# Kernel tuning notes

Hardware: AMD Instinct MI355X
Metric: run time of the kernel (lower is better)

The kernel has to match this reference:

```python
import jax, jax.numpy as jnp
import numpy as np

B, S, D, H = 2, 2048, 1024, 16
HD = D // H  # 64


def setup_inputs() -> dict:
    key = jax.random.key(0)
    ks = jax.random.split(key, 10)
    inp = {
        "queries": jax.random.normal(ks[0], (B, S, D), dtype=jnp.float32),
        "keys": jax.random.normal(ks[1], (B, S, D), dtype=jnp.float32),
        "values": jax.random.normal(ks[2], (B, S, D), dtype=jnp.float32),
        "attention_mask": jax.random.randint(ks[3], (B, S), 0, 2, dtype=jnp.int32),
        # Linear params (torch nn.Linear: y = x @ W.T + b), scaled like default init
        "Wq": jax.random.normal(ks[4], (D, D), dtype=jnp.float32) / np.sqrt(D),
        "bq": jnp.zeros((D,), dtype=jnp.float32),
        "Wk": jax.random.normal(ks[5], (D, D), dtype=jnp.float32) / np.sqrt(D),
        "bk": jnp.zeros((D,), dtype=jnp.float32),
        "Wv": jax.random.normal(ks[6], (D, D), dtype=jnp.float32) / np.sqrt(D),
        "bv": jnp.zeros((D,), dtype=jnp.float32),
    }
    return inp


def _split_heads(x):
    # torch.chunk along last dim + stack(dim=1) == reshape + transpose
    b, s, d = x.shape
    return x.reshape(b, s, H, HD).transpose(0, 2, 1, 3)  # [B,H,S,hd]


def reference(queries, keys, values, attention_mask, Wq, bq, Wk, bk, Wv, bv):
    q = jax.nn.relu(queries @ Wq.T + bq)
    k = jax.nn.relu(keys @ Wk.T + bk)
    v = jax.nn.relu(values @ Wv.T + bv)
    qh, kh, vh = _split_heads(q), _split_heads(k), _split_heads(v)
    score = jnp.einsum("bhqd,bhkd->bhqk", qh, kh) / jnp.sqrt(jnp.float32(HD))
    # enc mask: [B,1,S,1] broadcast over key dim — masks whole query rows where mask==0
    row_mask = (attention_mask == 0)[:, None, :, None]
    score = jnp.where(row_mask, jnp.float32(-1e9), score)
    attn = jax.nn.softmax(score, axis=-1)
    a = jnp.einsum("bhqk,bhkd->bhqd", attn, vh)  # [B,H,S,hd]
    # faithful to original: permute(0,1,3,2) then reshape to (B,S,D)
    a = a.transpose(0, 1, 3, 2).reshape(q.shape[0], q.shape[1], q.shape[2])
    return a + queries
```

## Files before the change

### kernel.cpp

```cpp
#include <hip/hip_runtime.h>
#include <hip/hip_bf16.h>

#define DEV __device__ __forceinline__

typedef __attribute__((ext_vector_type(8))) short short8;
typedef __attribute__((ext_vector_type(4))) float f32x4;

#define MFMA16(a, b, c) __builtin_amdgcn_mfma_f32_16x16x32_bf16((a), (b), (c), 0, 0, 0)

static constexpr int B_ = 2, S_ = 2048, D_ = 1024, H_ = 16, HD_ = 64;
static constexpr long NX = (long)B_ * S_ * D_;
static constexpr long NW = (long)D_ * D_;

DEV short f2bf(float f) {
    __hip_bfloat16 h = __float2bfloat16(f);
    union { __hip_bfloat16 hh; short s; } u;
    u.hh = h;
    return u.s;
}

DEV float bf2f(short s) {
    union { float f; unsigned u; } x;
    x.u = ((unsigned)(unsigned short)s) << 16;
    return x.f;
}

DEV short8 ld8(const short* p) { return *(const short8*)p; }

DEV void gld16(const short* g, short* l) {
    __builtin_amdgcn_global_load_lds(
        (const __attribute__((address_space(1))) unsigned int*)g,
        (__attribute__((address_space(3))) unsigned int*)l, 16, 0, 0);
}

__global__ __launch_bounds__(256) void convert_all(
    const float* __restrict__ q, const float* __restrict__ k, const float* __restrict__ v,
    const float* __restrict__ wq, const float* __restrict__ wk, const float* __restrict__ wv,
    short* __restrict__ qb, short* __restrict__ kb, short* __restrict__ vb,
    short* __restrict__ wqb, short* __restrict__ wkb, short* __restrict__ wvb) {
    long tid = (long)blockIdx.x * 256 + threadIdx.x;
    long e = tid * 4;
    const float* src; short* dst; long off;
    if      (e < NX)            { src = q;  dst = qb;  off = e; }
    else if (e < 2*NX)          { src = k;  dst = kb;  off = e - NX; }
    else if (e < 3*NX)          { src = v;  dst = vb;  off = e - 2*NX; }
    else if (e < 3*NX + NW)     { src = wq; dst = wqb; off = e - 3*NX; }
    else if (e < 3*NX + 2*NW)   { src = wk; dst = wkb; off = e - 3*NX - NW; }
    else                        { src = wv; dst = wvb; off = e - 3*NX - 2*NW; }
    float4 f = *(const float4*)(src + off);
    short4 o;
    o.x = f2bf(f.x); o.y = f2bf(f.y); o.z = f2bf(f.z); o.w = f2bf(f.w);
    *(short4*)(dst + off) = o;
}

__global__ __launch_bounds__(256) void gemm_bias_relu(
    const short* __restrict__ X0, const short* __restrict__ X1, const short* __restrict__ X2,
    const short* __restrict__ W0, const short* __restrict__ W1, const short* __restrict__ W2,
    const float* __restrict__ b0, const float* __restrict__ b1, const float* __restrict__ b2,
    short* __restrict__ O0, short* __restrict__ O1, short* __restrict__ O2) {
    __shared__ short As[2][128 * 32];
    __shared__ short Bs[2][128 * 32];

    const int z = blockIdx.z;
    const short* X   = (z == 0) ? X0 : (z == 1) ? X1 : X2;
    const short* W   = (z == 0) ? W0 : (z == 1) ? W1 : W2;
    const float* bia = (z == 0) ? b0 : (z == 1) ? b1 : b2;
    short*       Out = (z == 0) ? O0 : (z == 1) ? O1 : O2;

    const int tid  = threadIdx.x;
    const int wid  = tid >> 6;
    const int lane = tid & 63;
    const int id   = lane & 15;
    const int quad = lane >> 4;
    const int m0 = blockIdx.y * 128;
    const int n0 = blockIdx.x * 128;
    const int wm = (wid >> 1) * 64;
    const int wn = (wid & 1) * 64;

    const short* Ag0 = X + (long)(m0 + wid * 32 + (lane >> 2)) * D_ + (lane & 3) * 8;
    const short* Bg0 = W + (long)(n0 + wid * 32 + (lane >> 2)) * D_ + (lane & 3) * 8;
    const int offW = wid * 1024;

    f32x4 acc[4][4] = {};

    gld16(Ag0,            &As[0][offW]);
    gld16(Ag0 + 16 * D_,  &As[0][offW + 512]);
    gld16(Bg0,            &Bs[0][offW]);
    gld16(Bg0 + 16 * D_,  &Bs[0][offW + 512]);

    for (int kk = 0; kk < D_; kk += 32) {
        const int cur = (kk >> 5) & 1;
        __syncthreads();
        if (kk + 32 < D_) {
            const int nxt = cur ^ 1;
            gld16(Ag0 + kk + 32,            &As[nxt][offW]);
            gld16(Ag0 + 16 * D_ + kk + 32,  &As[nxt][offW + 512]);
            gld16(Bg0 + kk + 32,            &Bs[nxt][offW]);
            gld16(Bg0 + 16 * D_ + kk + 32,  &Bs[nxt][offW + 512]);
        }

        short8 af[4], bf[4];
#pragma unroll
        for (int i = 0; i < 4; i++) af[i] = ld8(&As[cur][(wm + 16*i + id) * 32 + quad * 8]);
#pragma unroll
        for (int j = 0; j < 4; j++) bf[j] = ld8(&Bs[cur][(wn + 16*j + id) * 32 + quad * 8]);
#pragma unroll
        for (int i = 0; i < 4; i++)
#pragma unroll
            for (int j = 0; j < 4; j++)
                acc[i][j] = MFMA16(af[i], bf[j], acc[i][j]);
    }

#pragma unroll
    for (int j = 0; j < 4; j++) {
        int col = n0 + wn + 16*j + id;
        float bj = bia[col];
#pragma unroll
        for (int i = 0; i < 4; i++) {
#pragma unroll
            for (int r = 0; r < 4; r++) {
                int row = m0 + wm + 16*i + quad*4 + r;
                float val = fmaxf(acc[i][j][r] + bj, 0.f);
                Out[(long)row * D_ + col] = f2bf(val);
            }
        }
    }
}

__global__ __launch_bounds__(256) void transpose_v(const short* __restrict__ Vp,
                                                   short* __restrict__ VT) {
    __shared__ short tile[64 * 64];
    const int bh = blockIdx.y;
    const int b = bh >> 4, h = bh & 15;
    const int s0 = blockIdx.x * 64;
    const int t = threadIdx.x;
#pragma unroll
    for (int it = 0; it < 2; it++) {
        int row = (t >> 3) + 32 * it;
        int u   = t & 7;
        short8 d = ld8(Vp + (long)(b * S_ + s0 + row) * D_ + h * HD_ + u * 8);
        *(short8*)(&tile[row * 64 + (u ^ ((row >> 3) & 7)) * 8]) = d;
    }
    __syncthreads();
#pragma unroll
    for (int it = 0; it < 2; it++) {
        int e  = (t >> 3) + 32 * it;
        int sb = (t & 7) * 8;
        short8 o;
#pragma unroll
        for (int u = 0; u < 8; u++) {
            int row = sb + u;
            o[u] = tile[row * 64 + (((e >> 3) ^ ((row >> 3) & 7)) * 8) + (e & 7)];
        }
        *(short8*)(VT + ((long)bh * HD_ + e) * S_ + s0 + sb) = o;
    }
}

__global__ __launch_bounds__(256, 2) void attention(
    const short* __restrict__ Qb, const short* __restrict__ Kb,
    const short* __restrict__ VT, const int* __restrict__ mask,
    const float* __restrict__ queries, float* __restrict__ out) {
    __shared__ short Ks[2][64 * 64];
    __shared__ short Vs[2][64 * 64];
    __shared__ short pl[4][2 * 16 * 72];

    const int tid  = threadIdx.x;
    const int wid  = tid >> 6;
    const int lane = tid & 63;
    const int id   = lane & 15;
    const int quad = lane >> 4;

    const int bid = blockIdx.x;
    const int qb_ = bid & 15;
    const int h   = (bid >> 4) & 15;
    const int b   = bid >> 8;
    const int q0  = qb_ * 128 + wid * 32;

    short8 qf[2][2];
#pragma unroll
    for (int g = 0; g < 2; g++) {
        const short* qbase = Qb + (long)(b * S_ + q0 + g * 16 + id) * D_ + h * HD_ + quad * 8;
        short8 f0 = ld8(qbase);
        short8 f1 = ld8(qbase + 32);
        const float qsc = mask[b * S_ + q0 + g * 16 + id] ? 0.125f : 0.f;
#pragma unroll
        for (int i = 0; i < 8; i++) {
            f0[i] = f2bf(bf2f(f0[i]) * qsc);
            f1[i] = f2bf(bf2f(f1[i]) * qsc);
        }
        qf[g][0] = f0; qf[g][1] = f1;
    }

    const int srow = wid * 16 + (lane >> 3);
    const int su   = (lane & 7) ^ (srow & 7);
    const short* kg0 = Kb + ((long)b * S_ + srow) * D_ + h * HD_ + su * 8;
    const short* vg0 = VT + (((long)(b * H_ + h) * HD_) + srow) * S_ + su * 8;
    short* plw = pl[wid];

    const int swz = id & 7;

    float l4[2][4] = {};
    f32x4 o[2][4] = {};

    gld16(kg0,            &Ks[0][wid * 1024]);
    gld16(kg0 + 8 * D_,   &Ks[0][wid * 1024 + 512]);
    gld16(vg0,            &Vs[0][wid * 1024]);
    gld16(vg0 + 8 * S_,   &Vs[0][wid * 1024 + 512]);

    for (int c0 = 0; c0 < S_; c0 += 64) {
        const int cur = (c0 >> 6) & 1;
        __syncthreads();
        if (c0 + 64 < S_) {
            const int nxt = cur ^ 1;
            const long cg = (long)(c0 + 64);
            gld16(kg0 + cg * D_,           &Ks[nxt][wid * 1024]);
            gld16(kg0 + cg * D_ + 8 * D_,  &Ks[nxt][wid * 1024 + 512]);
            gld16(vg0 + cg,                &Vs[nxt][wid * 1024]);
            gld16(vg0 + cg + 8 * S_,       &Vs[nxt][wid * 1024 + 512]);
        }

        f32x4 s[2][4];
#pragma unroll
        for (int g = 0; g < 2; g++)
#pragma unroll
            for (int t = 0; t < 4; t++) s[g][t] = (f32x4){0.f, 0.f, 0.f, 0.f};
#pragma unroll
        for (int t = 0; t < 4; t++) {
            short8 a0 = ld8(&Ks[cur][(16*t + id) * 64 + ((quad    ) ^ swz) * 8]);
            short8 a1 = ld8(&Ks[cur][(16*t + id) * 64 + ((quad ^ 4) ^ swz) * 8]);
            s[0][t] = MFMA16(a0, qf[0][0], s[0][t]);
            s[0][t] = MFMA16(a1, qf[0][1], s[0][t]);
            s[1][t] = MFMA16(a0, qf[1][0], s[1][t]);
            s[1][t] = MFMA16(a1, qf[1][1], s[1][t]);
        }

#pragma unroll
        for (int g = 0; g < 2; g++) {
            short* plg = plw + g * (16 * 72);
#pragma unroll
            for (int t = 0; t < 4; t++) {
                float p0 = __expf(s[g][t][0]);
                float p1 = __expf(s[g][t][1]);
                float p2 = __expf(s[g][t][2]);
                float p3 = __expf(s[g][t][3]);
                l4[g][0] += p0; l4[g][1] += p1; l4[g][2] += p2; l4[g][3] += p3;
                short4 w4;
                w4.x = f2bf(p0); w4.y = f2bf(p1); w4.z = f2bf(p2); w4.w = f2bf(p3);
                *(short4*)(&plg[id * 72 + 16 * t + quad * 4]) = w4;
            }
        }
        short8 pf[2][2];
#pragma unroll
        for (int g = 0; g < 2; g++) {
            short* plg = plw + g * (16 * 72);
            pf[g][0] = ld8(&plg[id * 72 + quad * 8]);
            pf[g][1] = ld8(&plg[id * 72 + 32 + quad * 8]);
        }

#pragma unroll
        for (int j2 = 0; j2 < 4; j2++) {
#pragma unroll
            for (int kh = 0; kh < 2; kh++) {
                short8 va = ld8(&Vs[cur][(16*j2 + id) * 64 + (((kh << 2) + quad) ^ swz) * 8]);
                o[0][j2] = MFMA16(va, pf[0][kh], o[0][j2]);
                o[1][j2] = MFMA16(va, pf[1][kh], o[1][j2]);
            }
        }
    }

    const long obase = (long)b * (S_ * D_) + (long)h * (HD_ * S_);
#pragma unroll
    for (int g = 0; g < 2; g++) {
        float l = l4[g][0] + l4[g][1] + l4[g][2] + l4[g][3];
        l += __shfl_xor(l, 16);
        l += __shfl_xor(l, 32);
        const float linv = 1.f / l;
#pragma unroll
        for (int j2 = 0; j2 < 4; j2++) {
#pragma unroll
            for (int r = 0; r < 4; r++) {
                int dim = 16 * j2 + quad * 4 + r;
                long idx = obase + (long)dim * S_ + q0 + g * 16 + id;
                out[idx] = o[g][j2][r] * linv + queries[idx];
            }
        }
    }
}

extern "C" void kernel_launch(void* const* d_in, const int* in_sizes, int n_in,
                              void* d_out, int out_size, void* d_ws, size_t ws_size,
                              hipStream_t stream) {
    const float* queries = (const float*)d_in[0];
    const float* keys    = (const float*)d_in[1];
    const float* values  = (const float*)d_in[2];
    const int*   mask    = (const int*)d_in[3];
    const float* Wq = (const float*)d_in[4];
    const float* bq = (const float*)d_in[5];
    const float* Wk = (const float*)d_in[6];
    const float* bk = (const float*)d_in[7];
    const float* Wv = (const float*)d_in[8];
    const float* bv = (const float*)d_in[9];
    float* out = (float*)d_out;

    short* ws  = (short*)d_ws;
    short* qb  = ws;
    short* kb  = qb  + NX;
    short* vb  = kb  + NX;
    short* wqb = vb  + NX;
    short* wkb = wqb + NW;
    short* wvb = wkb + NW;
    short* Q   = wvb + NW;
    short* K   = Q   + NX;
    short* Vp  = K   + NX;
    short* VT  = Vp  + NX;

    convert_all<<<15360, 256, 0, stream>>>(queries, keys, values, Wq, Wk, Wv,
                                           qb, kb, vb, wqb, wkb, wvb);
    gemm_bias_relu<<<dim3(8, 32, 3), 256, 0, stream>>>(qb, kb, vb, wqb, wkb, wvb,
                                                       bq, bk, bv, Q, K, Vp);
    transpose_v<<<dim3(32, 32), 256, 0, stream>>>(Vp, VT);
    attention<<<512, 256, 0, stream>>>(Q, K, VT, mask, queries, out);
}
```

Measured before the change: 206.8 us.

## Use two waves per attention block, each handling 64 queries with register-cached K/V

Halves the attention block to 128 threads, so each wave processes four 16-row query groups instead of two. K and V fragments are loaded from shared memory once per chunk into registers and reused across all four groups, which cuts LDS reads per FLOP. Each wave now issues four K/V tile loads per chunk instead of two. Register pressure rises (16 output accumulators plus the cached fragments), and there are fewer waves per block to hide latency.

```diff
diff --git a/kernel.cpp b/kernel.cpp
--- a/kernel.cpp
+++ b/kernel.cpp
@@ -156,13 +156,13 @@
     }
 }
 
-__global__ __launch_bounds__(256, 2) void attention(
+__global__ __launch_bounds__(128, 2) void attention(
     const short* __restrict__ Qb, const short* __restrict__ Kb,
     const short* __restrict__ VT, const int* __restrict__ mask,
     const float* __restrict__ queries, float* __restrict__ out) {
     __shared__ short Ks[2][64 * 64];
     __shared__ short Vs[2][64 * 64];
-    __shared__ short pl[4][2 * 16 * 72];
+    __shared__ short pl[2][2][16 * 72];
 
     const int tid  = threadIdx.x;
     const int wid  = tid >> 6;
@@ -174,11 +174,11 @@
     const int qb_ = bid & 15;
     const int h   = (bid >> 4) & 15;
     const int b   = bid >> 8;
-    const int q0  = qb_ * 128 + wid * 32;
-
-    short8 qf[2][2];
-#pragma unroll
-    for (int g = 0; g < 2; g++) {
+    const int q0  = qb_ * 128 + wid * 64;
+
+    short8 qf[4][2];
+#pragma unroll
+    for (int g = 0; g < 4; g++) {
         const short* qbase = Qb + (long)(b * S_ + q0 + g * 16 + id) * D_ + h * HD_ + quad * 8;
         short8 f0 = ld8(qbase);
         short8 f1 = ld8(qbase + 32);
@@ -191,21 +191,22 @@
         qf[g][0] = f0; qf[g][1] = f1;
     }
 
-    const int srow = wid * 16 + (lane >> 3);
+    const int srow = wid * 32 + (lane >> 3);
     const int su   = (lane & 7) ^ (srow & 7);
     const short* kg0 = Kb + ((long)b * S_ + srow) * D_ + h * HD_ + su * 8;
     const short* vg0 = VT + (((long)(b * H_ + h) * HD_) + srow) * S_ + su * 8;
-    short* plw = pl[wid];
 
     const int swz = id & 7;
 
-    float l4[2][4] = {};
-    f32x4 o[2][4] = {};
-
-    gld16(kg0,            &Ks[0][wid * 1024]);
-    gld16(kg0 + 8 * D_,   &Ks[0][wid * 1024 + 512]);
-    gld16(vg0,            &Vs[0][wid * 1024]);
-    gld16(vg0 + 8 * S_,   &Vs[0][wid * 1024 + 512]);
+    f32x4 l4 = {0.f, 0.f, 0.f, 0.f};
+    float lg[4] = {0.f, 0.f, 0.f, 0.f};
+    f32x4 o[4][4] = {};
+
+#pragma unroll
+    for (int m = 0; m < 4; m++) {
+        gld16(kg0 + (long)(8 * m) * D_, &Ks[0][wid * 2048 + m * 512]);
+        gld16(vg0 + (long)(8 * m) * S_, &Vs[0][wid * 2048 + m * 512]);
+    }
 
     for (int c0 = 0; c0 < S_; c0 += 64) {
         const int cur = (c0 >> 6) & 1;
@@ -213,65 +214,65 @@
         if (c0 + 64 < S_) {
             const int nxt = cur ^ 1;
             const long cg = (long)(c0 + 64);
-            gld16(kg0 + cg * D_,           &Ks[nxt][wid * 1024]);
-            gld16(kg0 + cg * D_ + 8 * D_,  &Ks[nxt][wid * 1024 + 512]);
-            gld16(vg0 + cg,                &Vs[nxt][wid * 1024]);
-            gld16(vg0 + cg + 8 * S_,       &Vs[nxt][wid * 1024 + 512]);
-        }
-
-        f32x4 s[2][4];
-#pragma unroll
-        for (int g = 0; g < 2; g++)
-#pragma unroll
-            for (int t = 0; t < 4; t++) s[g][t] = (f32x4){0.f, 0.f, 0.f, 0.f};
+#pragma unroll
+            for (int m = 0; m < 4; m++) {
+                gld16(kg0 + (cg + 8 * m) * D_, &Ks[nxt][wid * 2048 + m * 512]);
+                gld16(vg0 + cg + (long)(8 * m) * S_, &Vs[nxt][wid * 2048 + m * 512]);
+            }
+        }
+
+        short8 ka[4][2], va[4][2];
 #pragma unroll
         for (int t = 0; t < 4; t++) {
-            short8 a0 = ld8(&Ks[cur][(16*t + id) * 64 + ((quad    ) ^ swz) * 8]);
-            short8 a1 = ld8(&Ks[cur][(16*t + id) * 64 + ((quad ^ 4) ^ swz) * 8]);
-            s[0][t] = MFMA16(a0, qf[0][0], s[0][t]);
-            s[0][t] = MFMA16(a1, qf[0][1], s[0][t]);
-            s[1][t] = MFMA16(a0, qf[1][0], s[1][t]);
-            s[1][t] = MFMA16(a1, qf[1][1], s[1][t]);
-        }
-
-#pragma unroll
-        for (int g = 0; g < 2; g++) {
-            short* plg = plw + g * (16 * 72);
+            ka[t][0] = ld8(&Ks[cur][(16*t + id) * 64 + ((quad    ) ^ swz) * 8]);
+            ka[t][1] = ld8(&Ks[cur][(16*t + id) * 64 + ((quad ^ 4) ^ swz) * 8]);
+        }
+#pragma unroll
+        for (int j2 = 0; j2 < 4; j2++) {
+            va[j2][0] = ld8(&Vs[cur][(16*j2 + id) * 64 + ((quad    ) ^ swz) * 8]);
+            va[j2][1] = ld8(&Vs[cur][(16*j2 + id) * 64 + ((quad ^ 4) ^ swz) * 8]);
+        }
+
+#pragma unroll
+        for (int g = 0; g < 4; g++) {
+            f32x4 s[4];
+#pragma unroll
+            for (int t = 0; t < 4; t++) s[t] = (f32x4){0.f, 0.f, 0.f, 0.f};
 #pragma unroll
             for (int t = 0; t < 4; t++) {
-                float p0 = __expf(s[g][t][0]);
-                float p1 = __expf(s[g][t][1]);
-                float p2 = __expf(s[g][t][2]);
-                float p3 = __expf(s[g][t][3]);
-                l4[g][0] += p0; l4[g][1] += p1; l4[g][2] += p2; l4[g][3] += p3;
+                s[t] = MFMA16(ka[t][0], qf[g][0], s[t]);
+                s[t] = MFMA16(ka[t][1], qf[g][1], s[t]);
+            }
+
+            short* plg = &pl[wid][g & 1][0];
+            float ls = 0.f;
+#pragma unroll
+            for (int t = 0; t < 4; t++) {
+                float p0 = __expf(s[t][0]);
+                float p1 = __expf(s[t][1]);
+                float p2 = __expf(s[t][2]);
+                float p3 = __expf(s[t][3]);
+                ls += (p0 + p1) + (p2 + p3);
                 short4 w4;
                 w4.x = f2bf(p0); w4.y = f2bf(p1); w4.z = f2bf(p2); w4.w = f2bf(p3);
                 *(short4*)(&plg[id * 72 + 16 * t + quad * 4]) = w4;
             }
-        }
-        short8 pf[2][2];
-#pragma unroll
-        for (int g = 0; g < 2; g++) {
-            short* plg = plw + g * (16 * 72);
-            pf[g][0] = ld8(&plg[id * 72 + quad * 8]);
-            pf[g][1] = ld8(&plg[id * 72 + 32 + quad * 8]);
-        }
-
-#pragma unroll
-        for (int j2 = 0; j2 < 4; j2++) {
-#pragma unroll
-            for (int kh = 0; kh < 2; kh++) {
-                short8 va = ld8(&Vs[cur][(16*j2 + id) * 64 + (((kh << 2) + quad) ^ swz) * 8]);
-                o[0][j2] = MFMA16(va, pf[0][kh], o[0][j2]);
-                o[1][j2] = MFMA16(va, pf[1][kh], o[1][j2]);
+            lg[g] += ls;
+            short8 pf0 = ld8(&plg[id * 72 + quad * 8]);
+            short8 pf1 = ld8(&plg[id * 72 + 32 + quad * 8]);
+
+#pragma unroll
+            for (int j2 = 0; j2 < 4; j2++) {
+                o[g][j2] = MFMA16(va[j2][0], pf0, o[g][j2]);
+                o[g][j2] = MFMA16(va[j2][1], pf1, o[g][j2]);
             }
         }
     }
 
     const long obase = (long)b * (S_ * D_) + (long)h * (HD_ * S_);
 #pragma unroll
-    for (int g = 0; g < 2; g++) {
-        float l = l4[g][0] + l4[g][1] + l4[g][2] + l4[g][3];
+    for (int g = 0; g < 4; g++) {
+        float l = lg[g];
         l += __shfl_xor(l, 16);
         l += __shfl_xor(l, 32);
         const float linv = 1.f / l;
@@ -319,5 +320,5 @@
     gemm_bias_relu<<<dim3(8, 32, 3), 256, 0, stream>>>(qb, kb, vb, wqb, wkb, wvb,
                                                        bq, bk, bv, Q, K, Vp);
     transpose_v<<<dim3(32, 32), 256, 0, stream>>>(Vp, VT);
-    attention<<<512, 256, 0, stream>>>(Q, K, VT, mask, queries, out);
-}
+    attention<<<512, 128, 0, stream>>>(Q, K, VT, mask, queries, out);
+}
```

Result: slower. 230.9 us (+11.7%).
